# Kernel optimization log

Hardware: AMD Instinct MI355X
Metric: run time of the kernel (lower is better)

Reference implementation:

```python
import jax, jax.numpy as jnp
import numpy as np

N1, N2, N3 = 200000, 40000, 10000
E1, E2 = 640000, 160000
IN, HID, OUT = 128, 256, 64


def setup_inputs() -> dict:
    key = jax.random.key(0)
    ks = jax.random.split(key, 12)
    s = lambda fan_in: 1.0 / np.sqrt(fan_in)
    return {
        "x": jax.random.normal(ks[0], (N1, IN), dtype=jnp.float32),
        "src1": jax.random.randint(ks[1], (E1,), 0, N1, dtype=jnp.int32),
        "dst1": jax.random.randint(ks[2], (E1,), 0, N2, dtype=jnp.int32),
        "src2": jax.random.randint(ks[3], (E2,), 0, N2, dtype=jnp.int32),
        "dst2": jax.random.randint(ks[4], (E2,), 0, N3, dtype=jnp.int32),
        "n2": N2,
        "n3": N3,
        "W1l": jax.random.uniform(ks[5], (HID, IN), jnp.float32, -s(IN), s(IN)),
        "W1r": jax.random.uniform(ks[6], (HID, IN), jnp.float32, -s(IN), s(IN)),
        "b1": jax.random.uniform(ks[7], (HID,), jnp.float32, -s(IN), s(IN)),
        "W2l": jax.random.uniform(ks[8], (OUT, HID), jnp.float32, -s(HID), s(HID)),
        "W2r": jax.random.uniform(ks[9], (OUT, HID), jnp.float32, -s(HID), s(HID)),
        "b2": jax.random.uniform(ks[10], (OUT,), jnp.float32, -s(HID), s(HID)),
    }


def _sage_conv(x_src, x_tgt, src, dst, n_tgt, Wl, Wr, b):
    # mean aggregation of source-node messages into target nodes
    msg = x_src[src]                                        # [E, d]
    agg = jax.ops.segment_sum(msg, dst, num_segments=n_tgt)  # [n_tgt, d]
    cnt = jax.ops.segment_sum(jnp.ones(src.shape, x_src.dtype), dst,
                              num_segments=n_tgt)
    mean = agg / jnp.maximum(cnt, 1.0)[:, None]
    # lin_l(mean) + bias + lin_r(x_tgt)   (PyG SAGEConv, root_weight=True)
    return mean @ Wl.T + b + x_tgt @ Wr.T


def reference(x, src1, dst1, src2, dst2, n2, n3,
              W1l, W1r, b1, W2l, W2r, b2):
    h = _sage_conv(x, x[:n2], src1, dst1, n2, W1l, W1r, b1)  # [N2, HID]
    h = jax.nn.relu(h)  # dropout omitted (eval mode)
    out = _sage_conv(h, h[:n3], src2, dst2, n3, W2l, W2r, b2)  # [N3, OUT]
    return jax.nn.log_softmax(out, axis=-1)
```

## Files before the change

kernel.cpp:

```cpp
#include <hip/hip_runtime.h>

static constexpr int N1  = 200000;
static constexpr int N2  = 40000;
static constexpr int N3  = 10000;
static constexpr int IND = 128;
static constexpr int HID = 256;
static constexpr int OUTD = 64;

using f32x4  = __attribute__((ext_vector_type(4))) float;
using bf16x8 = __attribute__((ext_vector_type(8))) short;

__device__ __forceinline__ unsigned short f2bf(float f) {
    unsigned int u = __float_as_uint(f);
    u += 0x7FFFu + ((u >> 16) & 1u);
    return (unsigned short)(u >> 16);
}
__device__ __forceinline__ float bf2f(unsigned short u) {
    return __uint_as_float((unsigned int)u << 16);
}

static constexpr int NW1g = HID * 2 * IND / 4;
static constexpr int NW2g = OUTD * 2 * HID / 4;
static constexpr int NX_BIG   = N1 * IND / 8;
static constexpr int NX_SMALL = N2 * 32;

__global__ __launch_bounds__(256) void p1_kernel(
    const float* __restrict__ x, unsigned short* __restrict__ xdst, int big,
    const float* __restrict__ W1l, const float* __restrict__ W1r,
    unsigned short* __restrict__ Wb1,
    const float* __restrict__ W2l, const float* __restrict__ W2r,
    unsigned short* __restrict__ W2b,
    const int* __restrict__ dst1, int E1,
    const int* __restrict__ dst2, int E2,
    int* __restrict__ deg1, int* __restrict__ deg2) {
    int i = blockIdx.x * blockDim.x + threadIdx.x;
    const int NX = big ? NX_BIG : NX_SMALL;
    if (i < NX) {
        if (big) {
            const float4* p = reinterpret_cast<const float4*>(x + (size_t)i * 8);
            float4 v0 = p[0], v1 = p[1];
            uint4 u;
            u.x = (unsigned int)f2bf(v0.x) | ((unsigned int)f2bf(v0.y) << 16);
            u.y = (unsigned int)f2bf(v0.z) | ((unsigned int)f2bf(v0.w) << 16);
            u.z = (unsigned int)f2bf(v1.x) | ((unsigned int)f2bf(v1.y) << 16);
            u.w = (unsigned int)f2bf(v1.z) | ((unsigned int)f2bf(v1.w) << 16);
            *reinterpret_cast<uint4*>(xdst + (size_t)i * 8) = u;
        } else {
            int row = i >> 5, c4 = (i & 31) * 4;
            float4 v = *reinterpret_cast<const float4*>(x + (size_t)row * IND + c4);
            unsigned int lo = (unsigned int)f2bf(v.x) | ((unsigned int)f2bf(v.y) << 16);
            unsigned int hi = (unsigned int)f2bf(v.z) | ((unsigned int)f2bf(v.w) << 16);
            *reinterpret_cast<uint2*>(xdst + (size_t)row * 256 + 128 + c4) =
                make_uint2(lo, hi);
        }
    } else if ((i -= NX) < E1 + E2) {
        if (i < E1) atomicAdd(&deg1[dst1[i]], 1);
        else        atomicAdd(&deg2[dst2[i - E1]], 1);
    } else if ((i -= (E1 + E2)) < NW1g) {
        int j = i >> 6, k4 = (i & 63) * 4;
        const float* src = (k4 < IND) ? (W1l + (size_t)j * IND + k4)
                                      : (W1r + (size_t)j * IND + (k4 - IND));
        float4 v = *reinterpret_cast<const float4*>(src);
        *reinterpret_cast<ushort4*>(Wb1 + (size_t)j * 256 + k4) =
            make_ushort4(f2bf(v.x), f2bf(v.y), f2bf(v.z), f2bf(v.w));
    } else if ((i -= NW1g) < NW2g) {
        int j = i >> 7, k4 = (i & 127) * 4;
        const float* src = (k4 < HID) ? (W2l + (size_t)j * HID + k4)
                                      : (W2r + (size_t)j * HID + (k4 - HID));
        float4 v = *reinterpret_cast<const float4*>(src);
        *reinterpret_cast<ushort4*>(W2b + (size_t)j * 512 + k4) =
            make_ushort4(f2bf(v.x), f2bf(v.y), f2bf(v.z), f2bf(v.w));
    }
}

__device__ __forceinline__ int block_excl_scan(int s, int* wl) {
    __syncthreads();
    const int t = threadIdx.x, lane = t & 63, wid = t >> 6;
    int incl = s;
#pragma unroll
    for (int o = 1; o < 64; o <<= 1) {
        int u = __shfl_up(incl, o);
        if (lane >= o) incl += u;
    }
    if (lane == 63) wl[wid] = incl;
    __syncthreads();
    if (t < 16) {
        int v = wl[t], iv = v;
#pragma unroll
        for (int o = 1; o < 16; o <<= 1) {
            int u = __shfl_up(iv, o);
            if (t >= o) iv += u;
        }
        wl[t] = iv - v;
    }
    __syncthreads();
    return wl[wid] + incl - s;
}

template <int PER>
__device__ __forceinline__ void scan_seg(const int* __restrict__ deg,
                                         int* __restrict__ rs,
                                         int n4, int* wl) {
    const int t = threadIdx.x;
    int4 v[PER];
    int s = 0;
#pragma unroll
    for (int i = 0; i < PER; ++i) {
        int idx = t * PER + i;
        if (idx < n4) {
            v[i] = reinterpret_cast<const int4*>(deg)[idx];
            s += v[i].x + v[i].y + v[i].z + v[i].w;
        } else {
            v[i] = make_int4(0, 0, 0, 0);
        }
    }
    int run = block_excl_scan(s, wl);
#pragma unroll
    for (int i = 0; i < PER; ++i) {
        int idx = t * PER + i;
        if (idx < n4) {
            reinterpret_cast<int4*>(rs)[idx] =
                make_int4(run, run + v[i].x, run + v[i].x + v[i].y,
                          run + v[i].x + v[i].y + v[i].z);
            run += v[i].x + v[i].y + v[i].z + v[i].w;
        }
    }
}

__global__ __launch_bounds__(1024) void scan_fused_kernel(
    const int* __restrict__ deg1, int* __restrict__ rowstart1,
    const int* __restrict__ deg2, int* __restrict__ rowstart2) {
    __shared__ int wl[16];
    scan_seg<10>(deg1, rowstart1, N2 / 4, wl);
    scan_seg<3>(deg2, rowstart2, N3 / 4, wl);
}

__global__ void fill_both_kernel(
    const int* __restrict__ src1, const int* __restrict__ dst1, int E1,
    const int* __restrict__ rowstart1, int* __restrict__ cursor1,
    int* __restrict__ csr1,
    const int* __restrict__ src2, const int* __restrict__ dst2, int E2,
    const int* __restrict__ rowstart2, int* __restrict__ cursor2,
    int* __restrict__ csr2) {
    int i = blockIdx.x * blockDim.x + threadIdx.x;
    if (i < E1) {
        int d = dst1[i];
        int p = atomicAdd(&cursor1[d], 1);
        csr1[rowstart1[d] + p] = src1[i];
    } else if (i - E1 < E2) {
        int j = i - E1;
        int d = dst2[j];
        int p = atomicAdd(&cursor2[d], 1);
        csr2[rowstart2[d] + p] = src2[j];
    }
}

__global__ __launch_bounds__(256) void gather1b_kernel(
    const unsigned short* __restrict__ xb, const int* __restrict__ csr,
    const int* __restrict__ rowstart, const int* __restrict__ deg,
    unsigned short* __restrict__ meanb) {
    const int node = blockIdx.x * 4 + (threadIdx.x >> 6);
    const int lane = threadIdx.x & 63;
    const int beg = rowstart[node];
    const int n   = deg[node];
    const unsigned short* __restrict__ xcol = xb + lane * 2;
    float a0 = 0.f, a1 = 0.f, b0 = 0.f, b1 = 0.f;
    float c0 = 0.f, c1 = 0.f, d0 = 0.f, d1 = 0.f;
    int e = 0;
    for (; e + 3 < n; e += 4) {
        int s0 = csr[beg + e],     s1 = csr[beg + e + 1];
        int s2 = csr[beg + e + 2], s3 = csr[beg + e + 3];
        unsigned int v0 = *reinterpret_cast<const unsigned int*>(xcol + (size_t)s0 * IND);
        unsigned int v1 = *reinterpret_cast<const unsigned int*>(xcol + (size_t)s1 * IND);
        unsigned int v2 = *reinterpret_cast<const unsigned int*>(xcol + (size_t)s2 * IND);
        unsigned int v3 = *reinterpret_cast<const unsigned int*>(xcol + (size_t)s3 * IND);
        a0 += bf2f((unsigned short)v0); a1 += bf2f((unsigned short)(v0 >> 16));
        b0 += bf2f((unsigned short)v1); b1 += bf2f((unsigned short)(v1 >> 16));
        c0 += bf2f((unsigned short)v2); c1 += bf2f((unsigned short)(v2 >> 16));
        d0 += bf2f((unsigned short)v3); d1 += bf2f((unsigned short)(v3 >> 16));
    }
    for (; e < n; ++e) {
        int s0 = csr[beg + e];
        unsigned int v0 = *reinterpret_cast<const unsigned int*>(xcol + (size_t)s0 * IND);
        a0 += bf2f((unsigned short)v0); a1 += bf2f((unsigned short)(v0 >> 16));
    }
    const float inv = (n > 0) ? 1.0f / (float)n : 0.0f;
    const float m0 = ((a0 + b0) + (c0 + d0)) * inv;
    const float m1 = ((a1 + b1) + (c1 + d1)) * inv;
    unsigned int packed = (unsigned int)f2bf(m0) | ((unsigned int)f2bf(m1) << 16);
    *reinterpret_cast<unsigned int*>(meanb + (size_t)node * IND + lane * 2) = packed;
}

__global__ __launch_bounds__(256) void gather1_kernel(
    const float* __restrict__ x, const int* __restrict__ csr,
    const int* __restrict__ rowstart, const int* __restrict__ deg,
    unsigned short* __restrict__ A1b) {
    const int node = blockIdx.x * 4 + (threadIdx.x >> 6);
    const int lane = threadIdx.x & 63;
    const int beg = rowstart[node];
    const int n   = deg[node];
    float2 acc0 = make_float2(0.f, 0.f), acc1 = make_float2(0.f, 0.f);
    int e = 0;
    for (; e + 1 < n; e += 2) {
        int s0 = csr[beg + e];
        int s1 = csr[beg + e + 1];
        float2 v0 = *reinterpret_cast<const float2*>(x + (size_t)s0 * IND + lane * 2);
        float2 v1 = *reinterpret_cast<const float2*>(x + (size_t)s1 * IND + lane * 2);
        acc0.x += v0.x; acc0.y += v0.y;
        acc1.x += v1.x; acc1.y += v1.y;
    }
    if (e < n) {
        int s0 = csr[beg + e];
        float2 v0 = *reinterpret_cast<const float2*>(x + (size_t)s0 * IND + lane * 2);
        acc0.x += v0.x; acc0.y += v0.y;
    }
    const float inv = (n > 0) ? 1.0f / (float)n : 0.0f;
    unsigned int packed = (unsigned int)f2bf((acc0.x + acc1.x) * inv)
                        | ((unsigned int)f2bf((acc0.y + acc1.y) * inv) << 16);
    *reinterpret_cast<unsigned int*>(A1b + (size_t)node * 256 + lane * 2) = packed;
}

__global__ __launch_bounds__(256) void sage1_kernel(
    const unsigned short* __restrict__ Am, int sM,
    const unsigned short* __restrict__ Ax, int sX,
    const unsigned short* __restrict__ Wb,
    const float* __restrict__ b1,
    unsigned short* __restrict__ hb) {
    const int t    = threadIdx.x;
    const int wave = t >> 6;
    const int lane = t & 63;
    const int l15  = lane & 15;
    const int kh   = lane >> 4;
    const int wm   = wave >> 1;
    const int wn   = wave & 1;
    const int row0 = blockIdx.x * 64 + wm * 32;
    const int col0 = blockIdx.y * 128 + wn * 64;

    f32x4 acc[2][4];
#pragma unroll
    for (int m = 0; m < 2; ++m)
#pragma unroll
        for (int n = 0; n < 4; ++n)
            acc[m][n] = (f32x4){0.f, 0.f, 0.f, 0.f};

#pragma unroll
    for (int ks = 0; ks < 8; ++ks) {
        const unsigned short* __restrict__ Ab = (ks < 4) ? Am : Ax;
        const int sA = (ks < 4) ? sM : sX;
        const int k0 = (ks & 3) * 32 + kh * 8;
        bf16x8 a[2], b[4];
#pragma unroll
        for (int m = 0; m < 2; ++m)
            a[m] = *reinterpret_cast<const bf16x8*>(
                Ab + (size_t)(row0 + m * 16 + l15) * sA + k0);
#pragma unroll
        for (int n = 0; n < 4; ++n)
            b[n] = *reinterpret_cast<const bf16x8*>(
                Wb + (size_t)(col0 + n * 16 + l15) * 256 + ks * 32 + kh * 8);
#pragma unroll
        for (int m = 0; m < 2; ++m)
#pragma unroll
            for (int n = 0; n < 4; ++n)
                acc[m][n] = __builtin_amdgcn_mfma_f32_16x16x32_bf16(
                    a[m], b[n], acc[m][n], 0, 0, 0);
    }

#pragma unroll
    for (int m = 0; m < 2; ++m) {
        const int r0 = row0 + m * 16 + kh * 4;
#pragma unroll
        for (int n = 0; n < 4; ++n) {
            const int c = col0 + n * 16 + l15;
            const float bias = b1[c];
#pragma unroll
            for (int j = 0; j < 4; ++j)
                hb[(size_t)(r0 + j) * HID + c] =
                    f2bf(fmaxf(acc[m][n][j] + bias, 0.0f));
        }
    }
}

__global__ __launch_bounds__(256) void gather2_kernel(
    const unsigned short* __restrict__ hb, const int* __restrict__ csr,
    const int* __restrict__ rowstart, const int* __restrict__ deg,
    unsigned short* __restrict__ meanb) {
    const int node = blockIdx.x * 4 + (threadIdx.x >> 6);
    const int lane = threadIdx.x & 63;
    const int beg = rowstart[node];
    const int n   = deg[node];
    const unsigned short* __restrict__ hcol = hb + lane * 4;
    float acc0 = 0.f, acc1 = 0.f, acc2 = 0.f, acc3 = 0.f;
    int e = 0;
    for (; e + 3 < n; e += 4) {
        int s0 = csr[beg + e],     s1 = csr[beg + e + 1];
        int s2 = csr[beg + e + 2], s3 = csr[beg + e + 3];
        ushort4 v0 = *reinterpret_cast<const ushort4*>(hcol + (size_t)s0 * HID);
        ushort4 v1 = *reinterpret_cast<const ushort4*>(hcol + (size_t)s1 * HID);
        ushort4 v2 = *reinterpret_cast<const ushort4*>(hcol + (size_t)s2 * HID);
        ushort4 v3 = *reinterpret_cast<const ushort4*>(hcol + (size_t)s3 * HID);
        acc0 += (bf2f(v0.x) + bf2f(v1.x)) + (bf2f(v2.x) + bf2f(v3.x));
        acc1 += (bf2f(v0.y) + bf2f(v1.y)) + (bf2f(v2.y) + bf2f(v3.y));
        acc2 += (bf2f(v0.z) + bf2f(v1.z)) + (bf2f(v2.z) + bf2f(v3.z));
        acc3 += (bf2f(v0.w) + bf2f(v1.w)) + (bf2f(v2.w) + bf2f(v3.w));
    }
    for (; e < n; ++e) {
        int s0 = csr[beg + e];
        ushort4 v0 = *reinterpret_cast<const ushort4*>(hcol + (size_t)s0 * HID);
        acc0 += bf2f(v0.x); acc1 += bf2f(v0.y);
        acc2 += bf2f(v0.z); acc3 += bf2f(v0.w);
    }
    const float inv = (n > 0) ? 1.0f / (float)n : 0.0f;
    unsigned int lo = (unsigned int)f2bf(acc0 * inv)
                    | ((unsigned int)f2bf(acc1 * inv) << 16);
    unsigned int hi = (unsigned int)f2bf(acc2 * inv)
                    | ((unsigned int)f2bf(acc3 * inv) << 16);
    *reinterpret_cast<uint2*>(meanb + (size_t)node * HID + lane * 4) =
        make_uint2(lo, hi);
}

__global__ __launch_bounds__(256) void sage2_kernel(
    const unsigned short* __restrict__ hb,
    const unsigned short* __restrict__ meanb,
    const unsigned short* __restrict__ Wb,
    const float* __restrict__ b2,
    float* __restrict__ out) {
    const int t    = threadIdx.x;
    const int wave = t >> 6;
    const int lane = t & 63;
    const int l15  = lane & 15;
    const int kh   = lane >> 4;
    const int row0 = blockIdx.x * 64 + wave * 16;
    const int arow = min(row0 + l15, N3 - 1);

    f32x4 acc[4];
#pragma unroll
    for (int n = 0; n < 4; ++n) acc[n] = (f32x4){0.f, 0.f, 0.f, 0.f};

#pragma unroll
    for (int half = 0; half < 2; ++half) {
        const unsigned short* __restrict__ A = half ? hb : meanb;
#pragma unroll
        for (int ks = 0; ks < 8; ++ks) {
            const int k0 = ks * 32 + kh * 8;
            bf16x8 a = *reinterpret_cast<const bf16x8*>(
                A + (size_t)arow * HID + k0);
            bf16x8 b[4];
#pragma unroll
            for (int n = 0; n < 4; ++n)
                b[n] = *reinterpret_cast<const bf16x8*>(
                    Wb + (size_t)(n * 16 + l15) * 512 + half * 256 + k0);
#pragma unroll
            for (int n = 0; n < 4; ++n)
                acc[n] = __builtin_amdgcn_mfma_f32_16x16x32_bf16(
                    a, b[n], acc[n], 0, 0, 0);
        }
    }

    float v[4][4];
#pragma unroll
    for (int n = 0; n < 4; ++n) {
        const float bn = b2[n * 16 + l15];
#pragma unroll
        for (int j = 0; j < 4; ++j) v[n][j] = acc[n][j] + bn;
    }

#pragma unroll
    for (int j = 0; j < 4; ++j) {
        float mx = fmaxf(fmaxf(v[0][j], v[1][j]), fmaxf(v[2][j], v[3][j]));
#pragma unroll
        for (int o = 1; o <= 8; o <<= 1) mx = fmaxf(mx, __shfl_xor(mx, o));
        float sm = 0.f;
#pragma unroll
        for (int n = 0; n < 4; ++n) sm += __expf(v[n][j] - mx);
#pragma unroll
        for (int o = 1; o <= 8; o <<= 1) sm += __shfl_xor(sm, o);
        const float lse = mx + __logf(sm);
        const int r = row0 + kh * 4 + j;
        if (r < N3) {
#pragma unroll
            for (int n = 0; n < 4; ++n)
                out[(size_t)r * OUTD + n * 16 + l15] = v[n][j] - lse;
        }
    }
}

extern "C" void kernel_launch(void* const* d_in, const int* in_sizes, int n_in,
                              void* d_out, int out_size, void* d_ws, size_t ws_size,
                              hipStream_t stream) {
    const float* x    = (const float*)d_in[0];
    const int*   src1 = (const int*)d_in[1];
    const int*   dst1 = (const int*)d_in[2];
    const int*   src2 = (const int*)d_in[3];
    const int*   dst2 = (const int*)d_in[4];
    const float* W1l  = (const float*)d_in[7];
    const float* W1r  = (const float*)d_in[8];
    const float* b1   = (const float*)d_in[9];
    const float* W2l  = (const float*)d_in[10];
    const float* W2r  = (const float*)d_in[11];
    const float* b2   = (const float*)d_in[12];
    float* out = (float*)d_out;

    const int E1 = in_sizes[1];
    const int E2 = in_sizes[3];

    static constexpr size_t NEED_NEW = 85916608;
    const bool big = ws_size >= NEED_NEW;

    char* ws = (char*)d_ws;
    unsigned short *mean1b, *mean2b, *hb, *xb = nullptr, *A1b = nullptr;
    unsigned short *W2b, *Wb1;
    int *csr1, *csr2, *deg1, *cursor1, *deg2, *cursor2, *rowstart1, *rowstart2;
    char* z0;

    if (big) {
        mean1b   = (unsigned short*)(ws + 0);
        mean2b   = (unsigned short*)(ws + 0);
        hb       = (unsigned short*)(ws + 10240000);
        xb       = (unsigned short*)(ws + 30720000);
        csr1     = (int*)(ws + 81920000);
        csr2     = (int*)(ws + 84480000);
        deg1     = (int*)(ws + 85120000);
        cursor1  = (int*)(ws + 85280000);
        deg2     = (int*)(ws + 85440000);
        cursor2  = (int*)(ws + 85480000);
        rowstart1= (int*)(ws + 85520000);
        rowstart2= (int*)(ws + 85680000);
        W2b      = (unsigned short*)(ws + 85720000);
        Wb1      = (unsigned short*)(ws + 85785536);
        z0 = ws + 85120000;
    } else {
        A1b      = (unsigned short*)(ws + 0);
        mean1b   = nullptr;
        mean2b   = (unsigned short*)(ws + 0);
        hb       = (unsigned short*)(ws + 20480000);
        csr1     = (int*)(ws + 40960000);
        csr2     = (int*)(ws + 43520000);
        deg1     = (int*)(ws + 44160000);
        cursor1  = (int*)(ws + 44320000);
        deg2     = (int*)(ws + 44480000);
        cursor2  = (int*)(ws + 44520000);
        rowstart1= (int*)(ws + 44560000);
        rowstart2= (int*)(ws + 44720000);
        W2b      = (unsigned short*)(ws + 44760000);
        Wb1      = (unsigned short*)(ws + 44825536);
        z0 = ws + 44160000;
    }

    hipMemsetAsync(z0, 0, 400000, stream);

    {
        const int NX = big ? NX_BIG : NX_SMALL;
        const int total = NX + (E1 + E2) + NW1g + NW2g;
        p1_kernel<<<(total + 255) / 256, 256, 0, stream>>>(
            x, big ? xb : A1b, (int)big,
            W1l, W1r, Wb1, W2l, W2r, W2b,
            dst1, E1, dst2, E2, deg1, deg2);
    }

    scan_fused_kernel<<<1, 1024, 0, stream>>>(deg1, rowstart1, deg2, rowstart2);
    {
        int tot = E1 + E2;
        fill_both_kernel<<<(tot + 255) / 256, 256, 0, stream>>>(
            src1, dst1, E1, rowstart1, cursor1, csr1,
            src2, dst2, E2, rowstart2, cursor2, csr2);
    }

    if (big) {
        gather1b_kernel<<<N2 / 4, 256, 0, stream>>>(xb, csr1, rowstart1, deg1,
                                                    mean1b);
        dim3 grid(N2 / 64, HID / 128);
        sage1_kernel<<<grid, 256, 0, stream>>>(mean1b, IND, xb, IND, Wb1, b1, hb);
    } else {
        gather1_kernel<<<N2 / 4, 256, 0, stream>>>(x, csr1, rowstart1, deg1, A1b);
        dim3 grid(N2 / 64, HID / 128);
        sage1_kernel<<<grid, 256, 0, stream>>>(A1b, HID, A1b + 128, HID, Wb1,
                                               b1, hb);
    }

    gather2_kernel<<<N3 / 4, 256, 0, stream>>>(hb, csr2, rowstart2, deg2, mean2b);
    sage2_kernel<<<(N3 + 63) / 64, 256, 0, stream>>>(hb, mean2b, W2b, b2, out);
}
```

Baseline: 209.8 us.

## Fuse layer-1 gather with SAGE GEMM and split degree histogram into own kernel

Replaces the separate layer-1 mean-gather and sage1 GEMM with one 512-thread kernel. It gathers 64 node means into shared memory and then runs bf16 MFMA over the concatenated mean and root features to produce the ReLU output directly. This removes the global round-trip of the mean buffer and one launch. The degree histogram atomics are also moved out of the prep kernel into their own kernel. Risks include lower gather parallelism, since each wave now handles 8 nodes serially, and the GEMM no longer being overlapped across blocks.

```diff
diff --git a/kernel.cpp b/kernel.cpp
--- a/kernel.cpp
+++ b/kernel.cpp
@@ -24,15 +24,12 @@
 static constexpr int NX_BIG   = N1 * IND / 8;
 static constexpr int NX_SMALL = N2 * 32;
 
-__global__ __launch_bounds__(256) void p1_kernel(
+__global__ __launch_bounds__(256) void prep_kernel(
     const float* __restrict__ x, unsigned short* __restrict__ xdst, int big,
     const float* __restrict__ W1l, const float* __restrict__ W1r,
     unsigned short* __restrict__ Wb1,
     const float* __restrict__ W2l, const float* __restrict__ W2r,
-    unsigned short* __restrict__ W2b,
-    const int* __restrict__ dst1, int E1,
-    const int* __restrict__ dst2, int E2,
-    int* __restrict__ deg1, int* __restrict__ deg2) {
+    unsigned short* __restrict__ W2b) {
     int i = blockIdx.x * blockDim.x + threadIdx.x;
     const int NX = big ? NX_BIG : NX_SMALL;
     if (i < NX) {
@@ -53,10 +50,7 @@
             *reinterpret_cast<uint2*>(xdst + (size_t)row * 256 + 128 + c4) =
                 make_uint2(lo, hi);
         }
-    } else if ((i -= NX) < E1 + E2) {
-        if (i < E1) atomicAdd(&deg1[dst1[i]], 1);
-        else        atomicAdd(&deg2[dst2[i - E1]], 1);
-    } else if ((i -= (E1 + E2)) < NW1g) {
+    } else if ((i -= NX) < NW1g) {
         int j = i >> 6, k4 = (i & 63) * 4;
         const float* src = (k4 < IND) ? (W1l + (size_t)j * IND + k4)
                                       : (W1r + (size_t)j * IND + (k4 - IND));
@@ -71,6 +65,15 @@
         *reinterpret_cast<ushort4*>(W2b + (size_t)j * 512 + k4) =
             make_ushort4(f2bf(v.x), f2bf(v.y), f2bf(v.z), f2bf(v.w));
     }
+}
+
+__global__ void hist_both_kernel(const int* __restrict__ dst1, int E1,
+                                 const int* __restrict__ dst2, int E2,
+                                 int* __restrict__ deg1,
+                                 int* __restrict__ deg2) {
+    int i = blockIdx.x * blockDim.x + threadIdx.x;
+    if (i < E1) atomicAdd(&deg1[dst1[i]], 1);
+    else if (i - E1 < E2) atomicAdd(&deg2[dst2[i - E1]], 1);
 }
 
 __device__ __forceinline__ int block_excl_scan(int s, int* wl) {
@@ -155,40 +158,105 @@
     }
 }
 
-__global__ __launch_bounds__(256) void gather1b_kernel(
-    const unsigned short* __restrict__ xb, const int* __restrict__ csr,
-    const int* __restrict__ rowstart, const int* __restrict__ deg,
-    unsigned short* __restrict__ meanb) {
-    const int node = blockIdx.x * 4 + (threadIdx.x >> 6);
-    const int lane = threadIdx.x & 63;
-    const int beg = rowstart[node];
-    const int n   = deg[node];
+__global__ __launch_bounds__(512) void fused1_kernel(
+    const unsigned short* __restrict__ xb,
+    const int* __restrict__ csr, const int* __restrict__ rowstart,
+    const int* __restrict__ deg,
+    const unsigned short* __restrict__ Wb, const float* __restrict__ b1,
+    unsigned short* __restrict__ hb) {
+    constexpr int LST = 136;
+    __shared__ unsigned short Am[64 * LST];
+    const int t    = threadIdx.x;
+    const int w    = t >> 6;
+    const int lane = t & 63;
+    const int blk  = blockIdx.x * 64;
+
     const unsigned short* __restrict__ xcol = xb + lane * 2;
-    float a0 = 0.f, a1 = 0.f, b0 = 0.f, b1 = 0.f;
-    float c0 = 0.f, c1 = 0.f, d0 = 0.f, d1 = 0.f;
-    int e = 0;
-    for (; e + 3 < n; e += 4) {
-        int s0 = csr[beg + e],     s1 = csr[beg + e + 1];
-        int s2 = csr[beg + e + 2], s3 = csr[beg + e + 3];
-        unsigned int v0 = *reinterpret_cast<const unsigned int*>(xcol + (size_t)s0 * IND);
-        unsigned int v1 = *reinterpret_cast<const unsigned int*>(xcol + (size_t)s1 * IND);
-        unsigned int v2 = *reinterpret_cast<const unsigned int*>(xcol + (size_t)s2 * IND);
-        unsigned int v3 = *reinterpret_cast<const unsigned int*>(xcol + (size_t)s3 * IND);
-        a0 += bf2f((unsigned short)v0); a1 += bf2f((unsigned short)(v0 >> 16));
-        b0 += bf2f((unsigned short)v1); b1 += bf2f((unsigned short)(v1 >> 16));
-        c0 += bf2f((unsigned short)v2); c1 += bf2f((unsigned short)(v2 >> 16));
-        d0 += bf2f((unsigned short)v3); d1 += bf2f((unsigned short)(v3 >> 16));
-    }
-    for (; e < n; ++e) {
-        int s0 = csr[beg + e];
-        unsigned int v0 = *reinterpret_cast<const unsigned int*>(xcol + (size_t)s0 * IND);
-        a0 += bf2f((unsigned short)v0); a1 += bf2f((unsigned short)(v0 >> 16));
-    }
-    const float inv = (n > 0) ? 1.0f / (float)n : 0.0f;
-    const float m0 = ((a0 + b0) + (c0 + d0)) * inv;
-    const float m1 = ((a1 + b1) + (c1 + d1)) * inv;
-    unsigned int packed = (unsigned int)f2bf(m0) | ((unsigned int)f2bf(m1) << 16);
-    *reinterpret_cast<unsigned int*>(meanb + (size_t)node * IND + lane * 2) = packed;
+#pragma unroll 1
+    for (int r = w * 8; r < w * 8 + 8; ++r) {
+        const int node = blk + r;
+        const int beg = rowstart[node];
+        const int n   = deg[node];
+        float a0 = 0.f, a1 = 0.f, b0 = 0.f, b1v = 0.f;
+        float c0 = 0.f, c1 = 0.f, d0 = 0.f, d1v = 0.f;
+        int e = 0;
+        for (; e + 3 < n; e += 4) {
+            int s0 = csr[beg + e],     s1 = csr[beg + e + 1];
+            int s2 = csr[beg + e + 2], s3 = csr[beg + e + 3];
+            unsigned int v0 = *reinterpret_cast<const unsigned int*>(xcol + (size_t)s0 * IND);
+            unsigned int v1 = *reinterpret_cast<const unsigned int*>(xcol + (size_t)s1 * IND);
+            unsigned int v2 = *reinterpret_cast<const unsigned int*>(xcol + (size_t)s2 * IND);
+            unsigned int v3 = *reinterpret_cast<const unsigned int*>(xcol + (size_t)s3 * IND);
+            a0 += bf2f((unsigned short)v0); a1  += bf2f((unsigned short)(v0 >> 16));
+            b0 += bf2f((unsigned short)v1); b1v += bf2f((unsigned short)(v1 >> 16));
+            c0 += bf2f((unsigned short)v2); c1  += bf2f((unsigned short)(v2 >> 16));
+            d0 += bf2f((unsigned short)v3); d1v += bf2f((unsigned short)(v3 >> 16));
+        }
+        for (; e < n; ++e) {
+            int s0 = csr[beg + e];
+            unsigned int v0 = *reinterpret_cast<const unsigned int*>(xcol + (size_t)s0 * IND);
+            a0 += bf2f((unsigned short)v0); a1 += bf2f((unsigned short)(v0 >> 16));
+        }
+        const float inv = (n > 0) ? 1.0f / (float)n : 0.0f;
+        const float m0 = ((a0 + b0) + (c0 + d0)) * inv;
+        const float m1 = ((a1 + b1v) + (c1 + d1v)) * inv;
+        unsigned int packed = (unsigned int)f2bf(m0) | ((unsigned int)f2bf(m1) << 16);
+        *reinterpret_cast<unsigned int*>(&Am[r * LST + lane * 2]) = packed;
+    }
+    __syncthreads();
+
+    const int l15 = lane & 15;
+    const int kh  = lane >> 4;
+    const int wm  = w >> 2;
+    const int wn  = w & 3;
+    const int lr0 = wm * 32;
+    const int col0 = wn * 64;
+
+    f32x4 acc[2][4];
+#pragma unroll
+    for (int m = 0; m < 2; ++m)
+#pragma unroll
+        for (int n = 0; n < 4; ++n)
+            acc[m][n] = (f32x4){0.f, 0.f, 0.f, 0.f};
+
+#pragma unroll
+    for (int ks = 0; ks < 8; ++ks) {
+        const int k0 = (ks & 3) * 32 + kh * 8;
+        bf16x8 a[2], b[4];
+#pragma unroll
+        for (int m = 0; m < 2; ++m) {
+            if (ks < 4)
+                a[m] = *reinterpret_cast<const bf16x8*>(
+                    &Am[(lr0 + m * 16 + l15) * LST + k0]);
+            else
+                a[m] = *reinterpret_cast<const bf16x8*>(
+                    xb + (size_t)(blk + lr0 + m * 16 + l15) * IND + k0);
+        }
+#pragma unroll
+        for (int n = 0; n < 4; ++n)
+            b[n] = *reinterpret_cast<const bf16x8*>(
+                Wb + (size_t)(col0 + n * 16 + l15) * 256 + ks * 32 + kh * 8);
+#pragma unroll
+        for (int m = 0; m < 2; ++m)
+#pragma unroll
+            for (int n = 0; n < 4; ++n)
+                acc[m][n] = __builtin_amdgcn_mfma_f32_16x16x32_bf16(
+                    a[m], b[n], acc[m][n], 0, 0, 0);
+    }
+
+#pragma unroll
+    for (int m = 0; m < 2; ++m) {
+        const int r0 = blk + lr0 + m * 16 + kh * 4;
+#pragma unroll
+        for (int n = 0; n < 4; ++n) {
+            const int c = col0 + n * 16 + l15;
+            const float bias = b1[c];
+#pragma unroll
+            for (int j = 0; j < 4; ++j)
+                hb[(size_t)(r0 + j) * HID + c] =
+                    f2bf(fmaxf(acc[m][n][j] + bias, 0.0f));
+        }
+    }
 }
 
 __global__ __launch_bounds__(256) void gather1_kernel(
@@ -407,13 +475,12 @@
     const bool big = ws_size >= NEED_NEW;
 
     char* ws = (char*)d_ws;
-    unsigned short *mean1b, *mean2b, *hb, *xb = nullptr, *A1b = nullptr;
+    unsigned short *mean2b, *hb, *xb = nullptr, *A1b = nullptr;
     unsigned short *W2b, *Wb1;
     int *csr1, *csr2, *deg1, *cursor1, *deg2, *cursor2, *rowstart1, *rowstart2;
     char* z0;
 
     if (big) {
-        mean1b   = (unsigned short*)(ws + 0);
         mean2b   = (unsigned short*)(ws + 0);
         hb       = (unsigned short*)(ws + 10240000);
         xb       = (unsigned short*)(ws + 30720000);
@@ -430,7 +497,6 @@
         z0 = ws + 85120000;
     } else {
         A1b      = (unsigned short*)(ws + 0);
-        mean1b   = nullptr;
         mean2b   = (unsigned short*)(ws + 0);
         hb       = (unsigned short*)(ws + 20480000);
         csr1     = (int*)(ws + 40960000);
@@ -450,26 +516,26 @@
 
     {
         const int NX = big ? NX_BIG : NX_SMALL;
-        const int total = NX + (E1 + E2) + NW1g + NW2g;
-        p1_kernel<<<(total + 255) / 256, 256, 0, stream>>>(
+        const int total = NX + NW1g + NW2g;
+        prep_kernel<<<(total + 255) / 256, 256, 0, stream>>>(
             x, big ? xb : A1b, (int)big,
-            W1l, W1r, Wb1, W2l, W2r, W2b,
-            dst1, E1, dst2, E2, deg1, deg2);
-    }
-
-    scan_fused_kernel<<<1, 1024, 0, stream>>>(deg1, rowstart1, deg2, rowstart2);
+            W1l, W1r, Wb1, W2l, W2r, W2b);
+    }
+
     {
         int tot = E1 + E2;
+        hist_both_kernel<<<(tot + 255) / 256, 256, 0, stream>>>(
+            dst1, E1, dst2, E2, deg1, deg2);
+        scan_fused_kernel<<<1, 1024, 0, stream>>>(deg1, rowstart1,
+                                                  deg2, rowstart2);
         fill_both_kernel<<<(tot + 255) / 256, 256, 0, stream>>>(
             src1, dst1, E1, rowstart1, cursor1, csr1,
             src2, dst2, E2, rowstart2, cursor2, csr2);
     }
 
     if (big) {
-        gather1b_kernel<<<N2 / 4, 256, 0, stream>>>(xb, csr1, rowstart1, deg1,
-                                                    mean1b);
-        dim3 grid(N2 / 64, HID / 128);
-        sage1_kernel<<<grid, 256, 0, stream>>>(mean1b, IND, xb, IND, Wb1, b1, hb);
+        fused1_kernel<<<N2 / 64, 512, 0, stream>>>(xb, csr1, rowstart1, deg1,
+                                                   Wb1, b1, hb);
     } else {
         gather1_kernel<<<N2 / 4, 256, 0, stream>>>(x, csr1, rowstart1, deg1, A1b);
         dim3 grid(N2 / 64, HID / 128);
```

After: 240.4 us. 1.15x slower.
